# Kernel tuning notes

Measured on AMD Instinct MI355X. Metric: run time of the kernel, lower is better.

Reference implementation:

```python
import jax, jax.numpy as jnp
import numpy as np

# Static config matching init_kwargs
NUM_EXPERTS = 8
CAP_FACTOR = 1.0
MIN_CAP = 8


def setup_inputs() -> dict:
    key = jax.random.key(0)
    ks = jax.random.split(key, 10)
    G, S, D, H, E = 4, 4096, 1024, 4096, NUM_EXPERTS
    s = 0.02  # init stddev like nn.initializers.normal(0.02)
    return {
        "x": jax.random.normal(ks[0], (G, S, D), dtype=jnp.float32),
        "gate": jax.random.normal(ks[1], (D, E), dtype=jnp.float32) * s,
        "W1": jax.random.normal(ks[2], (E, D, H), dtype=jnp.float32) * s,
        "b1": jnp.zeros((E, H), dtype=jnp.float32),
        "W2": jax.random.normal(ks[3], (E, H, D), dtype=jnp.float32) * s,
        "b2": jnp.zeros((E, D), dtype=jnp.float32),
        "Ws1": jax.random.normal(ks[4], (D, H), dtype=jnp.float32) * s,
        "bs1": jnp.zeros((H,), dtype=jnp.float32),
        "Ws2": jax.random.normal(ks[5], (H, D), dtype=jnp.float32) * s,
        "bs2": jnp.zeros((D,), dtype=jnp.float32),
    }


def reference(x, gate, W1, b1, W2, b2, Ws1, bs1, Ws2, bs2):
    G, S, D = x.shape
    E = gate.shape[1]
    T = G * S
    capacity = max(MIN_CAP, int(CAP_FACTOR * T / E))  # static -> 2048

    # ---- Router (inference path: indices + scores, loss = 0) ----
    logits = jnp.einsum('gsd,de->gse', x, gate)           # (G,S,E)
    probs = jax.nn.softmax(logits, axis=-1)
    flat_probs = probs.transpose(2, 0, 1).reshape(E, T)    # (E,T)
    # capacity <= T here, so padding width is 0 (kept implicit)
    scores, token_idx = jax.lax.top_k(flat_probs, k=capacity)  # (E,C)
    scores = jnp.where(scores > -1e8, scores, 0.0)

    # ---- Routed experts: gather -> per-expert FFN (grouped GEMM) -> scatter-add
    flat_x = x.reshape(T, D)
    tok = flat_x[token_idx]                                # (E,C,D) gather
    h = jax.nn.gelu(jnp.einsum('ecd,edh->ech', tok, W1) + b1[:, None, :])
    out_tok = jnp.einsum('ech,ehd->ecd', h, W2) + b2[:, None, :]
    scaled = out_tok * scores[..., None]                   # weight by routing prob
    routed = jnp.zeros_like(flat_x).at[token_idx.reshape(-1)].add(
        scaled.reshape(E * capacity, D)).reshape(G, S, D)

    # ---- Shared expert (single FFN applied to all tokens) ----
    shared = jax.nn.gelu(jnp.einsum('gsd,dh->gsh', x, Ws1) + bs1)
    shared = jnp.einsum('gsh,hd->gsd', shared, Ws2) + bs2

    return routed + shared
```

## Files before the change

### kernel.cpp

```cpp
#include <hip/hip_runtime.h>
#include <hip/hip_bf16.h>

using bf16 = __hip_bfloat16;
typedef short v8s __attribute__((ext_vector_type(8)));
typedef float v4f __attribute__((ext_vector_type(4)));

#define NE 8
#define NT 16384
#define ND 1024
#define NH 4096
#define CAP 2048

__device__ __forceinline__ void load_lds16(const void* g, void* s) {
  __builtin_amdgcn_global_load_lds(
      (const __attribute__((address_space(1))) unsigned int*)g,
      (__attribute__((address_space(3))) unsigned int*)s, 16, 0, 0);
}

__device__ __forceinline__ float gelu_tanh(float x) {
  float u = 0.7978845608028654f * (x + 0.044715f * x * x * x);
  float e = __expf(2.0f * u);
  float t = 1.0f - 2.0f / (e + 1.0f);
  return 0.5f * x * (1.0f + t);
}

__global__ __launch_bounds__(256) void cvt_bf16(const float* __restrict__ s,
                                                bf16* __restrict__ d, int n) {
  for (int i = (blockIdx.x * 256 + threadIdx.x) * 4; i < n; i += gridDim.x * 1024) {
    float4 v = *(const float4*)(s + i);
    bf16 o[4];
    o[0] = __float2bfloat16(v.x); o[1] = __float2bfloat16(v.y);
    o[2] = __float2bfloat16(v.z); o[3] = __float2bfloat16(v.w);
    *(ushort4*)(d + i) = *(ushort4*)o;
  }
}

__global__ __launch_bounds__(256) void tcvt(const float* __restrict__ src,
                                            bf16* __restrict__ dst, int R, int C) {
  __shared__ float tile[32][33];
  size_t mo = (size_t)blockIdx.z * R * C;
  int c0 = blockIdx.x * 32, r0 = blockIdx.y * 32;
  int tx = threadIdx.x & 31, ty = threadIdx.x >> 5;
  for (int i = ty; i < 32; i += 8)
    tile[i][tx] = src[mo + (size_t)(r0 + i) * C + c0 + tx];
  __syncthreads();
  for (int i = ty; i < 32; i += 8)
    dst[mo + (size_t)(c0 + i) * R + r0 + tx] = __float2bfloat16(tile[tx][i]);
}

__global__ __launch_bounds__(256) void router_k(const float* __restrict__ x,
                                                const float* __restrict__ gate,
                                                float* __restrict__ probs) {
  int wave = threadIdx.x >> 6, lane = threadIdx.x & 63;
  int t = blockIdx.x * 4 + wave;
  const float* xr = x + (size_t)t * ND;
  double acc[NE];
#pragma unroll
  for (int e = 0; e < NE; e++) acc[e] = 0.0;
  for (int d = lane; d < ND; d += 64) {
    double xv = (double)xr[d];
    const float* g = gate + d * NE;
#pragma unroll
    for (int e = 0; e < NE; e++) acc[e] += xv * (double)g[e];
  }
#pragma unroll
  for (int e = 0; e < NE; e++) {
    double v = acc[e];
#pragma unroll
    for (int off = 32; off > 0; off >>= 1) v += __shfl_xor(v, off);
    acc[e] = v;
  }
  if (lane == 0) {
    float l[NE], m = -1e30f;
#pragma unroll
    for (int e = 0; e < NE; e++) { l[e] = (float)acc[e]; m = fmaxf(m, l[e]); }
    float p[NE], s = 0.f;
#pragma unroll
    for (int e = 0; e < NE; e++) { p[e] = expf(l[e] - m); s += p[e]; }
#pragma unroll
    for (int e = 0; e < NE; e++) probs[e * NT + t] = p[e] / s;
  }
}

__global__ __launch_bounds__(1024) void topk_k(const float* __restrict__ probs,
                                               unsigned* __restrict__ thr_key,
                                               int* __restrict__ needed) {
  int e = blockIdx.x;
  const float* p = probs + e * NT;
  __shared__ int hist[256];
  __shared__ unsigned s_pref;
  __shared__ int s_rank;
  unsigned prefix = 0;
  int rank = CAP;
  for (int rd = 0; rd < 4; rd++) {
    int shift = 24 - rd * 8;
    if (threadIdx.x < 256) hist[threadIdx.x] = 0;
    __syncthreads();
    unsigned mask = (rd == 0) ? 0u : (0xFFFFFFFFu << (shift + 8));
    for (int t = threadIdx.x; t < NT; t += 1024) {
      unsigned k = __float_as_uint(p[t]);
      if ((k & mask) == prefix) atomicAdd(&hist[(k >> shift) & 255], 1);
    }
    __syncthreads();
    if (threadIdx.x == 0) {
      int cum = 0, b = 255;
      for (;;) {
        int c = hist[b];
        if (cum + c >= rank || b == 0) break;
        cum += c; b--;
      }
      s_pref = prefix | ((unsigned)b << shift);
      s_rank = rank - cum;
    }
    __syncthreads();
    prefix = s_pref; rank = s_rank;
    __syncthreads();
  }
  if (threadIdx.x == 0) { thr_key[e] = prefix; needed[e] = rank; }
}

__global__ void zero_counters(int* p) {
  if (threadIdx.x < 2 * NE) p[threadIdx.x] = 0;
}

__global__ __launch_bounds__(256) void compact_k(const float* __restrict__ probs,
                                                 const unsigned* __restrict__ thr_key,
                                                 const int* __restrict__ needed,
                                                 int* __restrict__ cnt, int* __restrict__ eqc,
                                                 int* __restrict__ tok, float* __restrict__ scr) {
  int gid = blockIdx.x * 256 + threadIdx.x;
  int e = gid >> 14, t = gid & (NT - 1);
  float pv = probs[gid];
  unsigned k = __float_as_uint(pv);
  unsigned thr = thr_key[e];
  int nd = needed[e];
  bool gt = k > thr, eq = k == thr;
  unsigned long long mgt = __ballot(gt), meq = __ballot(eq);
  int lane = threadIdx.x & 63, wv = threadIdx.x >> 6;
  __shared__ int wcnt[2][4];
  __shared__ int base[2];
  if (lane == 0) { wcnt[0][wv] = __popcll(mgt); wcnt[1][wv] = __popcll(meq); }
  __syncthreads();
  if (threadIdx.x == 0) {
    int s0 = wcnt[0][0] + wcnt[0][1] + wcnt[0][2] + wcnt[0][3];
    int s1 = wcnt[1][0] + wcnt[1][1] + wcnt[1][2] + wcnt[1][3];
    base[0] = s0 ? atomicAdd(&cnt[e], s0) : 0;
    base[1] = s1 ? atomicAdd(&eqc[e], s1) : 0;
  }
  __syncthreads();
  unsigned long long lm = (1ull << lane) - 1ull;
  if (gt) {
    int p = __popcll(mgt & lm);
    for (int w = 0; w < wv; w++) p += wcnt[0][w];
    int slot = base[0] + p;
    tok[e * CAP + slot] = t; scr[e * CAP + slot] = pv;
  } else if (eq) {
    int q = base[1] + __popcll(meq & lm);
    for (int w = 0; w < wv; w++) q += wcnt[1][w];
    if (q < nd) {
      int slot = (CAP - nd) + q;
      tok[e * CAP + slot] = t; scr[e * CAP + slot] = pv;
    }
  }
}

#define BAR() __builtin_amdgcn_s_barrier()
#define SBAR0() __builtin_amdgcn_sched_barrier(0)

template <int MODE>
__global__ __launch_bounds__(512, 2) void gemm256(
    const bf16* __restrict__ A, int lda, const int* __restrict__ rowmap,
    const bf16* __restrict__ BT, long long bstride, int gshift,
    const float* __restrict__ bias, int bias_stride,
    int N, int K,
    bf16* __restrict__ outH, float* __restrict__ outF,
    const int* __restrict__ tok, const float* __restrict__ scr) {
  __shared__ __attribute__((aligned(16))) char lds[131072];
  const int tid = threadIdx.x;
  const int lane = tid & 63, wv = tid >> 6;
  const int wr = wv >> 2, wc = wv & 3;
  const int hw = blockIdx.y * gridDim.x + blockIdx.x;
  const int nwg = gridDim.x * gridDim.y;
  const int swz = (hw & 7) * (nwg >> 3) + (hw >> 3);
  const int m0 = (swz & 63) << 8;
  const int n0 = (swz >> 6) << 8;
  const int grp = m0 >> gshift;
  const bf16* Bp = BT + (size_t)grp * (size_t)bstride;
  const float* bp = bias + (size_t)grp * (size_t)bias_stride;
  const int nt = K >> 6;

  const int srow = tid >> 3;
  const int pc = tid & 7;
  const int gc = pc ^ (srow & 7);
  const bf16* srcA[4]; const bf16* srcB[4];
#pragma unroll
  for (int g = 0; g < 4; g++) {
    int am = m0 + g * 64 + srow;
    int ar = rowmap ? rowmap[am] : am;
    srcA[g] = A + (size_t)ar * lda + gc * 8;
    srcB[g] = Bp + (size_t)(n0 + g * 64 + srow) * K + gc * 8;
  }
  auto stageA = [&](int t, int h) {
    char* d = lds + ((t & 1) * 65536 + h * 16384) + tid * 16;
    load_lds16(srcA[h * 2 + 0] + (size_t)t * 64, d);
    load_lds16(srcA[h * 2 + 1] + (size_t)t * 64, d + 8192);
  };
  auto stageB = [&](int t, int h) {
    char* d = lds + ((t & 1) * 65536 + 32768 + h * 16384) + tid * 16;
    load_lds16(srcB[h * 2 + 0] + (size_t)t * 64, d);
    load_lds16(srcB[h * 2 + 1] + (size_t)t * 64, d + 8192);
  };

  const int fr = lane & 15, hi = lane >> 4;
  const int xr = fr & 7;
  const int cb0 = ((0 + hi) ^ xr) << 4;
  const int cb1 = ((4 + hi) ^ xr) << 4;
  const int arow = ((wr << 7) + fr) << 7;
  const int brow = ((wc << 6) + fr) << 7;

  v4f acc[8][4] = {};
  v8s a03[4][2], a47[4][2], b01[2][2], b23[2][2];

#define R_A03(BASE)                                                           \
  _Pragma("unroll") for (int mi = 0; mi < 4; mi++) {                          \
    a03[mi][0] = *(const v8s*)((BASE) + arow + mi * 2048 + cb0);              \
    a03[mi][1] = *(const v8s*)((BASE) + arow + mi * 2048 + cb1);              \
  }
#define R_A47(BASE)                                                           \
  _Pragma("unroll") for (int mi = 0; mi < 4; mi++) {                          \
    a47[mi][0] = *(const v8s*)((BASE) + arow + (4 + mi) * 2048 + cb0);        \
    a47[mi][1] = *(const v8s*)((BASE) + arow + (4 + mi) * 2048 + cb1);        \
  }
#define R_B01(BASE)                                                           \
  _Pragma("unroll") for (int ni = 0; ni < 2; ni++) {                          \
    b01[ni][0] = *(const v8s*)((BASE) + brow + ni * 2048 + cb0);              \
    b01[ni][1] = *(const v8s*)((BASE) + brow + ni * 2048 + cb1);              \
  }
#define R_B23(BASE)                                                           \
  _Pragma("unroll") for (int ni = 0; ni < 2; ni++) {                          \
    b23[ni][0] = *(const v8s*)((BASE) + brow + (2 + ni) * 2048 + cb0);        \
    b23[ni][1] = *(const v8s*)((BASE) + brow + (2 + ni) * 2048 + cb1);        \
  }
#define MFMA_Q(AB, BB, MOFF, NOFF)                                            \
  __builtin_amdgcn_s_setprio(1);                                              \
  _Pragma("unroll") for (int kk = 0; kk < 2; kk++)                            \
  _Pragma("unroll") for (int mi = 0; mi < 4; mi++)                            \
  _Pragma("unroll") for (int ni = 0; ni < 2; ni++)                            \
    acc[(MOFF) + mi][(NOFF) + ni] = __builtin_amdgcn_mfma_f32_16x16x32_bf16(  \
        AB[mi][kk], BB[ni][kk], acc[(MOFF) + mi][(NOFF) + ni], 0, 0, 0);      \
  __builtin_amdgcn_s_setprio(0);

  stageA(0, 0); stageA(0, 1); stageB(0, 0); stageB(0, 1);
  if (nt > 1) { stageB(1, 0); stageB(1, 1); }
  if (nt > 1) { asm volatile("s_waitcnt vmcnt(4)" ::: "memory"); }
  else        { asm volatile("s_waitcnt vmcnt(0)" ::: "memory"); }
  BAR();
  {
    const char* Ab0 = lds; const char* Bb0 = lds + 32768;
    R_A03(Ab0); R_B01(Bb0); R_B23(Bb0); R_A47(Ab0);
  }

  for (int t = 0; t < nt; ++t) {
    const char* AbN = lds + ((t + 1) & 1) * 65536;
    const char* BbN = AbN + 32768;
    asm volatile("s_waitcnt lgkmcnt(12)" ::: "memory"); SBAR0();
    MFMA_Q(a03, b01, 0, 0);
    if (t + 1 < nt) stageA(t + 1, 0);
    asm volatile("s_waitcnt lgkmcnt(8)" ::: "memory"); SBAR0();
    MFMA_Q(a03, b23, 0, 2);
    if (t + 1 < nt) stageA(t + 1, 1);
    BAR();
    asm volatile("s_waitcnt lgkmcnt(0)" ::: "memory"); SBAR0();
    MFMA_Q(a47, b01, 4, 0);
    if (t + 2 < nt) stageB(t + 2, 0);
    if (t + 2 < nt) stageB(t + 2, 1);
    if (t + 2 < nt) { asm volatile("s_waitcnt vmcnt(4)" ::: "memory"); }
    else            { asm volatile("s_waitcnt vmcnt(0)" ::: "memory"); }
    BAR();
    if (t + 1 < nt) { R_A03(AbN); R_B01(BbN); }
    MFMA_Q(a47, b23, 4, 2);
    if (t + 1 < nt) { R_B23(BbN); R_A47(AbN); }
  }
  asm volatile("s_waitcnt vmcnt(0) lgkmcnt(0)" ::: "memory");

  float bv[4];
#pragma unroll
  for (int ni = 0; ni < 4; ni++) bv[ni] = bp[n0 + (wc << 6) + ni * 16 + fr];
  const int rbase = m0 + (wr << 7) + (hi << 2);
#pragma unroll
  for (int mi = 0; mi < 8; mi++) {
#pragma unroll
    for (int r = 0; r < 4; r++) {
      int gm = rbase + mi * 16 + r;
      int trow = 0; float sv = 0.f;
      if (MODE == 2) { trow = tok[gm]; sv = scr[gm]; }
#pragma unroll
      for (int ni = 0; ni < 4; ni++) {
        int gn = n0 + (wc << 6) + ni * 16 + fr;
        float v = acc[mi][ni][r] + bv[ni];
        if (MODE == 0)      outH[(size_t)gm * N + gn] = __float2bfloat16(gelu_tanh(v));
        else if (MODE == 1) outF[(size_t)gm * N + gn] = v;
        else                atomicAdd(outF + (size_t)trow * N + gn, v * sv);
      }
    }
  }
}

extern "C" void kernel_launch(void* const* d_in, const int* in_sizes, int n_in,
                              void* d_out, int out_size, void* d_ws, size_t ws_size,
                              hipStream_t stream) {
  const float* x   = (const float*)d_in[0];
  const float* gate= (const float*)d_in[1];
  const float* W1  = (const float*)d_in[2];
  const float* b1  = (const float*)d_in[3];
  const float* W2  = (const float*)d_in[4];
  const float* b2  = (const float*)d_in[5];
  const float* Ws1 = (const float*)d_in[6];
  const float* bs1 = (const float*)d_in[7];
  const float* Ws2 = (const float*)d_in[8];
  const float* bs2 = (const float*)d_in[9];
  float* out = (float*)d_out;

  char* w = (char*)d_ws;
  size_t off = 0;
  auto alloc = [&](size_t bytes) {
    void* p = w + off;
    off = (off + bytes + 255) & ~(size_t)255;
    return p;
  };
  bf16* xb    = (bf16*)alloc((size_t)NT * ND * 2);
  bf16* w1T   = (bf16*)alloc((size_t)NE * NH * ND * 2);
  bf16* w2T   = (bf16*)alloc((size_t)NE * ND * NH * 2);
  bf16* ws1T  = (bf16*)alloc((size_t)NH * ND * 2);
  bf16* ws2T  = (bf16*)alloc((size_t)ND * NH * 2);
  bf16* h     = (bf16*)alloc((size_t)NT * NH * 2);
  float* probs= (float*)alloc((size_t)NE * NT * 4);
  unsigned* thr = (unsigned*)alloc(NE * 4);
  int* needed = (int*)alloc(NE * 4);
  int* cnt    = (int*)alloc(2 * NE * 4);
  int* eqc    = cnt + NE;
  int* tok    = (int*)alloc((size_t)NE * CAP * 4);
  float* scr  = (float*)alloc((size_t)NE * CAP * 4);
  if (off > ws_size) return;

  cvt_bf16<<<2048, 256, 0, stream>>>(x, xb, NT * ND);
  tcvt<<<dim3(NH / 32, ND / 32, NE), 256, 0, stream>>>(W1, w1T, ND, NH);
  tcvt<<<dim3(ND / 32, NH / 32, NE), 256, 0, stream>>>(W2, w2T, NH, ND);
  tcvt<<<dim3(NH / 32, ND / 32, 1), 256, 0, stream>>>(Ws1, ws1T, ND, NH);
  tcvt<<<dim3(ND / 32, NH / 32, 1), 256, 0, stream>>>(Ws2, ws2T, NH, ND);

  router_k<<<NT / 4, 256, 0, stream>>>(x, gate, probs);
  topk_k<<<NE, 1024, 0, stream>>>(probs, thr, needed);
  zero_counters<<<1, 64, 0, stream>>>(cnt);
  compact_k<<<NE * NT / 256, 256, 0, stream>>>(probs, thr, needed, cnt, eqc, tok, scr);

  gemm256<0><<<dim3(NH / 256, NT / 256), 512, 0, stream>>>(
      xb, ND, nullptr, ws1T, 0, 30, bs1, 0, NH, ND, h, nullptr, nullptr, nullptr);
  gemm256<1><<<dim3(ND / 256, NT / 256), 512, 0, stream>>>(
      h, NH, nullptr, ws2T, 0, 30, bs2, 0, ND, NH, nullptr, out, nullptr, nullptr);

  gemm256<0><<<dim3(NH / 256, NT / 256), 512, 0, stream>>>(
      xb, ND, tok, w1T, (long long)NH * ND, 11, b1, NH, NH, ND, h, nullptr, nullptr, nullptr);
  gemm256<2><<<dim3(ND / 256, NT / 256), 512, 0, stream>>>(
      h, NH, nullptr, w2T, (long long)ND * NH, 11, b2, ND, ND, NH, nullptr, out, tok, scr);
}
```

Before: 845.4 us.

## Quantize routed-expert first GEMM to int8 with per-row scales

Adds a per-row symmetric int8 quantization kernel for activations and the transposed W1 weights, plus a new int8 MFMA GEMM (16x16x64 i8) for the routed experts' first projection. The epilogue dequantizes with the row and column scales, adds bias and applies GELU. Counter zeroing is folded into topk_k, dropping one launch. This trades accuracy, since int8 rounding error lands in the expert hidden activations, and adds quantization passes over x and all of W1 on every call.

```diff
diff --git a/kernel.cpp b/kernel.cpp
--- a/kernel.cpp
+++ b/kernel.cpp
@@ -4,6 +4,7 @@
 using bf16 = __hip_bfloat16;
 typedef short v8s __attribute__((ext_vector_type(8)));
 typedef float v4f __attribute__((ext_vector_type(4)));
+typedef int v4i __attribute__((ext_vector_type(4)));
 
 #define NE 8
 #define NT 16384
@@ -48,6 +49,45 @@
     dst[mo + (size_t)(c0 + i) * R + r0 + tx] = __float2bfloat16(tile[tx][i]);
 }
 
+__global__ __launch_bounds__(256) void rowq_k(const bf16* __restrict__ in,
+                                              signed char* __restrict__ q,
+                                              float* __restrict__ sc, int nrows) {
+  int row = blockIdx.x * 4 + (threadIdx.x >> 6);
+  if (row >= nrows) return;
+  int lane = threadIdx.x & 63;
+  const ushort* r = (const ushort*)in + (size_t)row * 1024;
+  ushort4 u[4];
+  u[0] = *(const ushort4*)(r + lane * 8);
+  u[1] = *(const ushort4*)(r + lane * 8 + 4);
+  u[2] = *(const ushort4*)(r + 512 + lane * 8);
+  u[3] = *(const ushort4*)(r + 512 + lane * 8 + 4);
+  float f[16];
+#pragma unroll
+  for (int j = 0; j < 4; j++) {
+    f[j * 4 + 0] = __uint_as_float((unsigned)u[j].x << 16);
+    f[j * 4 + 1] = __uint_as_float((unsigned)u[j].y << 16);
+    f[j * 4 + 2] = __uint_as_float((unsigned)u[j].z << 16);
+    f[j * 4 + 3] = __uint_as_float((unsigned)u[j].w << 16);
+  }
+  float m = 0.f;
+#pragma unroll
+  for (int j = 0; j < 16; j++) m = fmaxf(m, fabsf(f[j]));
+#pragma unroll
+  for (int off = 32; off > 0; off >>= 1) m = fmaxf(m, __shfl_xor(m, off));
+  float inv = (m > 1e-30f) ? 127.0f / m : 0.0f;
+  int b[16];
+#pragma unroll
+  for (int j = 0; j < 16; j++) b[j] = (int)rintf(f[j] * inv);
+  int w[4];
+#pragma unroll
+  for (int j = 0; j < 4; j++)
+    w[j] = (b[j * 4] & 255) | ((b[j * 4 + 1] & 255) << 8) |
+           ((b[j * 4 + 2] & 255) << 16) | (b[j * 4 + 3] << 24);
+  *(int2*)(q + (size_t)row * 1024 + lane * 8) = make_int2(w[0], w[1]);
+  *(int2*)(q + (size_t)row * 1024 + 512 + lane * 8) = make_int2(w[2], w[3]);
+  if (lane == 0) sc[row] = m * (1.0f / 127.0f);
+}
+
 __global__ __launch_bounds__(256) void router_k(const float* __restrict__ x,
                                                 const float* __restrict__ gate,
                                                 float* __restrict__ probs) {
@@ -84,7 +124,8 @@
 
 __global__ __launch_bounds__(1024) void topk_k(const float* __restrict__ probs,
                                                unsigned* __restrict__ thr_key,
-                                               int* __restrict__ needed) {
+                                               int* __restrict__ needed,
+                                               int* __restrict__ cnt) {
   int e = blockIdx.x;
   const float* p = probs + e * NT;
   __shared__ int hist[256];
@@ -116,11 +157,10 @@
     prefix = s_pref; rank = s_rank;
     __syncthreads();
   }
-  if (threadIdx.x == 0) { thr_key[e] = prefix; needed[e] = rank; }
-}
-
-__global__ void zero_counters(int* p) {
-  if (threadIdx.x < 2 * NE) p[threadIdx.x] = 0;
+  if (threadIdx.x == 0) {
+    thr_key[e] = prefix; needed[e] = rank;
+    cnt[e] = 0; cnt[NE + e] = 0;
+  }
 }
 
 __global__ __launch_bounds__(256) void compact_k(const float* __restrict__ probs,
@@ -306,6 +346,138 @@
   }
 }
 
+__global__ __launch_bounds__(512, 2) void gemm256_q(
+    const signed char* __restrict__ A, const int* __restrict__ rowmap,
+    const signed char* __restrict__ BT,
+    const float* __restrict__ sxr, const float* __restrict__ swc,
+    const float* __restrict__ bias, bf16* __restrict__ outH) {
+  __shared__ __attribute__((aligned(16))) char lds[131072];
+  const int tid = threadIdx.x;
+  const int lane = tid & 63, wv = tid >> 6;
+  const int wr = wv >> 2, wc = wv & 3;
+  const int m0 = blockIdx.y << 8, n0 = blockIdx.x << 8;
+  const int grp = m0 >> 11;
+  const signed char* Bp = BT + (size_t)grp * ((size_t)NH * ND);
+  const float* bp = bias + grp * NH;
+  const float* swp = swc + grp * NH;
+  const int nt = ND >> 7;
+
+  const int srow = tid >> 3;
+  const int pc = tid & 7;
+  const int gc = pc ^ (srow & 7);
+  const signed char* srcA[4]; const signed char* srcB[4];
+#pragma unroll
+  for (int g = 0; g < 4; g++) {
+    int am = m0 + g * 64 + srow;
+    int ar = rowmap[am];
+    srcA[g] = A + (size_t)ar * ND + gc * 16;
+    srcB[g] = Bp + (size_t)(n0 + g * 64 + srow) * ND + gc * 16;
+  }
+  auto stageA = [&](int t, int h) {
+    char* d = lds + ((t & 1) * 65536 + h * 16384) + tid * 16;
+    load_lds16(srcA[h * 2 + 0] + (size_t)t * 128, d);
+    load_lds16(srcA[h * 2 + 1] + (size_t)t * 128, d + 8192);
+  };
+  auto stageB = [&](int t, int h) {
+    char* d = lds + ((t & 1) * 65536 + 32768 + h * 16384) + tid * 16;
+    load_lds16(srcB[h * 2 + 0] + (size_t)t * 128, d);
+    load_lds16(srcB[h * 2 + 1] + (size_t)t * 128, d + 8192);
+  };
+
+  const int fr = lane & 15, hi = lane >> 4;
+  const int xr = fr & 7;
+  const int cb0 = ((0 + hi) ^ xr) << 4;
+  const int cb1 = ((4 + hi) ^ xr) << 4;
+  const int arow = ((wr << 7) + fr) << 7;
+  const int brow = ((wc << 6) + fr) << 7;
+
+  v4i acc[8][4] = {};
+  v4i a03[4][2], a47[4][2], b01[2][2], b23[2][2];
+
+#define QR_A03(BASE)                                                          \
+  _Pragma("unroll") for (int mi = 0; mi < 4; mi++) {                          \
+    a03[mi][0] = *(const v4i*)((BASE) + arow + mi * 2048 + cb0);              \
+    a03[mi][1] = *(const v4i*)((BASE) + arow + mi * 2048 + cb1);              \
+  }
+#define QR_A47(BASE)                                                          \
+  _Pragma("unroll") for (int mi = 0; mi < 4; mi++) {                          \
+    a47[mi][0] = *(const v4i*)((BASE) + arow + (4 + mi) * 2048 + cb0);        \
+    a47[mi][1] = *(const v4i*)((BASE) + arow + (4 + mi) * 2048 + cb1);        \
+  }
+#define QR_B01(BASE)                                                          \
+  _Pragma("unroll") for (int ni = 0; ni < 2; ni++) {                          \
+    b01[ni][0] = *(const v4i*)((BASE) + brow + ni * 2048 + cb0);              \
+    b01[ni][1] = *(const v4i*)((BASE) + brow + ni * 2048 + cb1);              \
+  }
+#define QR_B23(BASE)                                                          \
+  _Pragma("unroll") for (int ni = 0; ni < 2; ni++) {                          \
+    b23[ni][0] = *(const v4i*)((BASE) + brow + (2 + ni) * 2048 + cb0);        \
+    b23[ni][1] = *(const v4i*)((BASE) + brow + (2 + ni) * 2048 + cb1);        \
+  }
+#define QMFMA_Q(AB, BB, MOFF, NOFF)                                           \
+  __builtin_amdgcn_s_setprio(1);                                              \
+  _Pragma("unroll") for (int kk = 0; kk < 2; kk++)                            \
+  _Pragma("unroll") for (int mi = 0; mi < 4; mi++)                            \
+  _Pragma("unroll") for (int ni = 0; ni < 2; ni++)                            \
+    acc[(MOFF) + mi][(NOFF) + ni] = __builtin_amdgcn_mfma_i32_16x16x64_i8(    \
+        AB[mi][kk], BB[ni][kk], acc[(MOFF) + mi][(NOFF) + ni], 0, 0, 0);      \
+  __builtin_amdgcn_s_setprio(0);
+
+  stageA(0, 0); stageA(0, 1); stageB(0, 0); stageB(0, 1);
+  stageB(1, 0); stageB(1, 1);
+  asm volatile("s_waitcnt vmcnt(4)" ::: "memory");
+  BAR();
+  {
+    const char* Ab0 = lds; const char* Bb0 = lds + 32768;
+    QR_A03(Ab0); QR_B01(Bb0); QR_B23(Bb0); QR_A47(Ab0);
+  }
+
+  for (int t = 0; t < nt; ++t) {
+    const char* AbN = lds + ((t + 1) & 1) * 65536;
+    const char* BbN = AbN + 32768;
+    asm volatile("s_waitcnt lgkmcnt(12)" ::: "memory"); SBAR0();
+    QMFMA_Q(a03, b01, 0, 0);
+    if (t + 1 < nt) stageA(t + 1, 0);
+    asm volatile("s_waitcnt lgkmcnt(8)" ::: "memory"); SBAR0();
+    QMFMA_Q(a03, b23, 0, 2);
+    if (t + 1 < nt) stageA(t + 1, 1);
+    BAR();
+    asm volatile("s_waitcnt lgkmcnt(0)" ::: "memory"); SBAR0();
+    QMFMA_Q(a47, b01, 4, 0);
+    if (t + 2 < nt) stageB(t + 2, 0);
+    if (t + 2 < nt) stageB(t + 2, 1);
+    if (t + 2 < nt) { asm volatile("s_waitcnt vmcnt(4)" ::: "memory"); }
+    else            { asm volatile("s_waitcnt vmcnt(0)" ::: "memory"); }
+    BAR();
+    if (t + 1 < nt) { QR_A03(AbN); QR_B01(BbN); }
+    QMFMA_Q(a47, b23, 4, 2);
+    if (t + 1 < nt) { QR_B23(BbN); QR_A47(AbN); }
+  }
+  asm volatile("s_waitcnt vmcnt(0) lgkmcnt(0)" ::: "memory");
+
+  float bv[4], swv[4];
+#pragma unroll
+  for (int ni = 0; ni < 4; ni++) {
+    int gn = n0 + (wc << 6) + ni * 16 + fr;
+    bv[ni] = bp[gn]; swv[ni] = swp[gn];
+  }
+  const int rbase = m0 + (wr << 7) + (hi << 2);
+#pragma unroll
+  for (int mi = 0; mi < 8; mi++) {
+#pragma unroll
+    for (int r = 0; r < 4; r++) {
+      int gm = rbase + mi * 16 + r;
+      float sxa = sxr[rowmap[gm]];
+#pragma unroll
+      for (int ni = 0; ni < 4; ni++) {
+        int gn = n0 + (wc << 6) + ni * 16 + fr;
+        float v = (float)acc[mi][ni][r] * (sxa * swv[ni]) + bv[ni];
+        outH[(size_t)gm * NH + gn] = __float2bfloat16(gelu_tanh(v));
+      }
+    }
+  }
+}
+
 extern "C" void kernel_launch(void* const* d_in, const int* in_sizes, int n_in,
                               void* d_out, int out_size, void* d_ws, size_t ws_size,
                               hipStream_t stream) {
@@ -334,6 +506,10 @@
   bf16* ws1T  = (bf16*)alloc((size_t)NH * ND * 2);
   bf16* ws2T  = (bf16*)alloc((size_t)ND * NH * 2);
   bf16* h     = (bf16*)alloc((size_t)NT * NH * 2);
+  signed char* xq  = (signed char*)alloc((size_t)NT * ND);
+  signed char* w1q = (signed char*)alloc((size_t)NE * NH * ND);
+  float* sx   = (float*)alloc((size_t)NT * 4);
+  float* sw1  = (float*)alloc((size_t)NE * NH * 4);
   float* probs= (float*)alloc((size_t)NE * NT * 4);
   unsigned* thr = (unsigned*)alloc(NE * 4);
   int* needed = (int*)alloc(NE * 4);
@@ -341,6 +517,7 @@
   int* eqc    = cnt + NE;
   int* tok    = (int*)alloc((size_t)NE * CAP * 4);
   float* scr  = (float*)alloc((size_t)NE * CAP * 4);
+  (void)alloc(65536);
   if (off > ws_size) return;
 
   cvt_bf16<<<2048, 256, 0, stream>>>(x, xb, NT * ND);
@@ -349,9 +526,11 @@
   tcvt<<<dim3(NH / 32, ND / 32, 1), 256, 0, stream>>>(Ws1, ws1T, ND, NH);
   tcvt<<<dim3(ND / 32, NH / 32, 1), 256, 0, stream>>>(Ws2, ws2T, NH, ND);
 
+  rowq_k<<<NT / 4, 256, 0, stream>>>(xb, xq, sx, NT);
+  rowq_k<<<NE * NH / 4, 256, 0, stream>>>(w1T, w1q, sw1, NE * NH);
+
   router_k<<<NT / 4, 256, 0, stream>>>(x, gate, probs);
-  topk_k<<<NE, 1024, 0, stream>>>(probs, thr, needed);
-  zero_counters<<<1, 64, 0, stream>>>(cnt);
+  topk_k<<<NE, 1024, 0, stream>>>(probs, thr, needed, cnt);
   compact_k<<<NE * NT / 256, 256, 0, stream>>>(probs, thr, needed, cnt, eqc, tok, scr);
 
   gemm256<0><<<dim3(NH / 256, NT / 256), 512, 0, stream>>>(
@@ -359,8 +538,8 @@
   gemm256<1><<<dim3(ND / 256, NT / 256), 512, 0, stream>>>(
       h, NH, nullptr, ws2T, 0, 30, bs2, 0, ND, NH, nullptr, out, nullptr, nullptr);
 
-  gemm256<0><<<dim3(NH / 256, NT / 256), 512, 0, stream>>>(
-      xb, ND, tok, w1T, (long long)NH * ND, 11, b1, NH, NH, ND, h, nullptr, nullptr, nullptr);
+  gemm256_q<<<dim3(NH / 256, NT / 256), 512, 0, stream>>>(
+      xq, tok, w1q, sx, sw1, b1, h);
   gemm256<2><<<dim3(ND / 256, NT / 256), 512, 0, stream>>>(
       h, NH, nullptr, w2T, (long long)ND * NH, 11, b2, ND, ND, NH, nullptr, out, tok, scr);
 }
```

Result: no change. 835.5 us (-1.2%).
